# Kernel tuning notes

Hardware: AMD Instinct MI355X
Metric: run time of the kernel (lower is better)

The kernel has to match this reference:

```python
import jax, jax.numpy as jnp
import numpy as np
from jax import lax

L = 2048        # leaves per tree
VOCAB = 50000
IN_DIM = 300
MEM = 150
HID = 50
NCLS = 5


def _balanced_tree(n_leaf):
    # children-before-parent topological order; node ids: [0, n_leaf) leaves,
    # [n_leaf, 2*n_leaf-1) internal, last id is the root's single child (ROOT is passthrough).
    level = list(range(n_leaf)); nid = n_leaf; lefts = []; rights = []
    while len(level) > 1:
        nxt = []
        for j in range(0, len(level) - 1, 2):
            lefts.append(level[j]); rights.append(level[j + 1]); nxt.append(nid); nid += 1
        if len(level) % 2:
            nxt.append(level[-1])
        level = nxt
    return np.asarray(lefts, np.int32), np.asarray(rights, np.int32)


def setup_inputs() -> dict:
    key = jax.random.key(0)
    ks = jax.random.split(key, 12)
    left, right = _balanced_tree(L)
    s = 0.05
    return {
        "l_tokens": jax.random.randint(ks[0], (L,), 0, VOCAB, dtype=jnp.int32),
        "r_tokens": jax.random.randint(ks[1], (L,), 0, VOCAB, dtype=jnp.int32),
        "left_idx": jnp.asarray(left),
        "right_idx": jnp.asarray(right),
        "emb": jax.random.normal(ks[2], (VOCAB, IN_DIM), jnp.float32) * s,
        "W_ioux": jax.random.normal(ks[3], (IN_DIM, 3 * MEM), jnp.float32) * s,
        "b_ioux": jnp.zeros((3 * MEM,), jnp.float32),
        "W_iouh": jax.random.normal(ks[4], (MEM, 3 * MEM), jnp.float32) * s,
        "b_iouh": jnp.zeros((3 * MEM,), jnp.float32),
        "W_fx": jax.random.normal(ks[5], (IN_DIM, MEM), jnp.float32) * s,
        "b_fx": jnp.zeros((MEM,), jnp.float32),
        "W_fh": jax.random.normal(ks[6], (MEM, MEM), jnp.float32) * s,
        "b_fh": jnp.zeros((MEM,), jnp.float32),
        "W_attn": jax.random.normal(ks[7], (2 * MEM, MEM), jnp.float32) * s,
        "b_attn": jnp.zeros((MEM,), jnp.float32),
        "W_wh": jax.random.normal(ks[8], (2 * MEM, HID), jnp.float32) * s,
        "b_wh": jnp.zeros((HID,), jnp.float32),
        "W_wp": jax.random.normal(ks[9], (HID, NCLS), jnp.float32) * s,
        "b_wp": jnp.zeros((NCLS,), jnp.float32),
    }


def _gates(iou):
    i, o, u = jnp.split(iou, 3, axis=-1)
    return jax.nn.sigmoid(i), jax.nn.sigmoid(o), jnp.tanh(u)


def _tree_lstm(tokens, left, right, emb, W_ioux, b_ioux, W_iouh, b_iouh, W_fh, b_fh):
    # Leaves (child_c = child_h = 0): iou = ioux(x) + iouh(0); fc term vanishes.
    x = emb[tokens]                                   # [L, in_dim]
    i, o, u = _gates(x @ W_ioux + b_ioux + b_iouh)
    c_leaf = i * u
    h_leaf = o * jnp.tanh(c_leaf)
    n_leaf = tokens.shape[0]
    N = 2 * n_leaf - 1
    C = jnp.zeros((N, MEM), x.dtype).at[:n_leaf].set(c_leaf)
    H = jnp.zeros((N, MEM), x.dtype).at[:n_leaf].set(h_leaf)

    # Internal nodes (inputs=None branch): iou = iouh(sum h_child); f_k = sigmoid(fh(h_k)).
    def step(carry, inp):
        C, H = carry
        k, li, ri = inp
        hl, hr = H[li], H[ri]
        i, o, u = _gates((hl + hr) @ W_iouh + b_iouh)
        fl = jax.nn.sigmoid(hl @ W_fh + b_fh)
        fr = jax.nn.sigmoid(hr @ W_fh + b_fh)
        c = i * u + fl * C[li] + fr * C[ri]
        h = o * jnp.tanh(c)
        return (C.at[k].set(c), H.at[k].set(h)), None

    ids = jnp.arange(n_leaf, N, dtype=jnp.int32)
    (C, H), _ = lax.scan(step, (C, H), (ids, left, right))
    return H  # [N, MEM]; H[-1] is the root hidden state (ROOT is passthrough)


def reference(l_tokens, r_tokens, left_idx, right_idx, emb, W_ioux, b_ioux, W_iouh, b_iouh, W_fx, b_fx, W_fh, b_fh, W_attn, b_attn, W_wh, b_wh, W_wp, b_wp):
    Hl = _tree_lstm(l_tokens, left_idx, right_idx, emb, W_ioux, b_ioux, W_iouh, b_iouh, W_fh, b_fh)
    Hr = _tree_lstm(r_tokens, left_idx, right_idx, emb, W_ioux, b_ioux, W_iouh, b_iouh, W_fh, b_fh)
    # Soft cross-attention over all node hidden states (torch code builds [Nr,Nl,m] beta;
    # here expressed as matmuls -- identical math).
    scores = Hl @ Hr.T                               # [Nl, Nr]
    beta_sum = jax.nn.softmax(scores, axis=1) @ Hr    # [Nl, MEM]
    alpha_sum = jax.nn.softmax(scores.T, axis=1) @ Hl  # [Nr, MEM]
    v_l = jnp.concatenate([Hl, beta_sum], axis=1) @ W_attn + b_attn
    v_r = jnp.concatenate([Hr, alpha_sum], axis=1) @ W_attn + b_attn
    lh = v_l[-1:]  # root hidden (root_idx is the root's matched row)
    rh = v_r[-1:]
    feats = jnp.concatenate([lh * rh, jnp.abs(lh - rh)], axis=1)
    hid = jax.nn.sigmoid(feats @ W_wh + b_wh)
    return jax.nn.log_softmax(hid @ W_wp + b_wp, axis=-1)  # [1, NCLS]
```

## Files before the change

### kernel.cpp

```cpp
#include <hip/hip_runtime.h>
#include <math.h>

#define LEAVES 2048
#define NN     4095
#define MEMD   150
#define IOUD   450
#define IND    300
#define STR    152
#define CT     4096


__device__ __forceinline__ float sigf(float x) { return 1.f / (1.f + expf(-x)); }

__global__ __launch_bounds__(640) void k_leaf(
    const int* __restrict__ ltok, const int* __restrict__ rtok,
    const float* __restrict__ emb, const float* __restrict__ Wx,
    const float* __restrict__ bx, const float* __restrict__ bh,
    float* __restrict__ C, float* __restrict__ H)
{
    __shared__ float xs[IND][8];
    __shared__ int   tok[8];
    __shared__ float pb[300][13];
    const int tree = blockIdx.y, t = threadIdx.x;
    const int leaf0 = blockIdx.x << 3;
    const int* toks = tree ? rtok : ltok;

    if (t < 8) tok[t] = toks[leaf0 + t];
    __syncthreads();
    if (t < 600) {
        int q = t >> 3, m = t & 7;
        float4 v = *(const float4*)(emb + (size_t)tok[m] * IND + 4 * q);
        xs[4*q+0][m] = v.x; xs[4*q+1][m] = v.y;
        xs[4*q+2][m] = v.z; xs[4*q+3][m] = v.w;
    }
    __syncthreads();

    const int kh = (t >= 320) ? 1 : 0;
    const int tt = t - 320 * kh;
    const bool act = (tt < 300);
    const int hf = (tt >= 150) ? 1 : 0;
    const int d  = tt - 150 * hf;
    const int m0 = hf * 4;

    float ai[4], ao[4], au[4];
    if (act) {
        if (kh == 0) {
            const float bi = bx[d]       + bh[d];
            const float bo = bx[d + 150] + bh[d + 150];
            const float bu = bx[d + 300] + bh[d + 300];
            #pragma unroll
            for (int m = 0; m < 4; ++m) { ai[m] = bi; ao[m] = bo; au[m] = bu; }
        } else {
            #pragma unroll
            for (int m = 0; m < 4; ++m) { ai[m] = 0.f; ao[m] = 0.f; au[m] = 0.f; }
        }
        const float* wp = Wx + d;
        const int kb = kh * 150;
        #pragma unroll 5
        for (int kk = 0; kk < 150; ++kk) {
            const int k = kb + kk;
            float wi = wp[k * IOUD];
            float wo = wp[k * IOUD + 150];
            float wu = wp[k * IOUD + 300];
            float4 x4 = *(const float4*)(&xs[k][m0]);
            float xv[4] = {x4.x, x4.y, x4.z, x4.w};
            #pragma unroll
            for (int m = 0; m < 4; ++m) {
                ai[m] = fmaf(xv[m], wi, ai[m]);
                ao[m] = fmaf(xv[m], wo, ao[m]);
                au[m] = fmaf(xv[m], wu, au[m]);
            }
        }
    }
    if (kh == 1 && act) {
        #pragma unroll
        for (int m = 0; m < 4; ++m) {
            pb[tt][3*m + 0] = ai[m];
            pb[tt][3*m + 1] = ao[m];
            pb[tt][3*m + 2] = au[m];
        }
    }
    __syncthreads();
    if (kh == 0 && act) {
        float* Ct = C + ((size_t)tree * CT + leaf0 + m0) * STR;
        float* Ht = H + ((size_t)tree * CT + leaf0 + m0) * STR;
        #pragma unroll
        for (int m = 0; m < 4; ++m) {
            float aiv = ai[m] + pb[tt][3*m + 0];
            float aov = ao[m] + pb[tt][3*m + 1];
            float auv = au[m] + pb[tt][3*m + 2];
            float c = sigf(aiv) * tanhf(auv);
            float h = sigf(aov) * tanhf(c);
            Ct[(size_t)m * STR + d] = c;
            Ht[(size_t)m * STR + d] = h;
        }
    }
}

__global__ __launch_bounds__(640) void k_lvl(
    const float* __restrict__ Wh, const float* __restrict__ bh,
    const float* __restrict__ Wf, const float* __restrict__ bf,
    float* __restrict__ C, float* __restrict__ H, int PB, int CB)
{
    __shared__ float buf[MEMD][8];
    __shared__ float pb[300][11];
    const int tree = blockIdx.y, t = threadIdx.x;
    const int p0 = blockIdx.x * 4;
    float* Ct = C + (size_t)tree * CT * STR;
    float* Ht = H + (size_t)tree * CT * STR;

    if (t < 600) {
        int m = t / 150, d2 = t - m * 150;
        int cc = CB + 2 * (p0 + m);
        float a = Ht[(size_t)cc * STR + d2];
        float b = Ht[(size_t)(cc + 1) * STR + d2];
        buf[d2][2*m + 0] = a + b;
        buf[d2][2*m + 1] = a;
    }
    __syncthreads();

    const int kh = (t >= 320) ? 1 : 0;
    const int tt = t - 320 * kh;
    const bool act = (tt < 300);
    const int hf = (tt >= 150) ? 1 : 0;
    const int d  = tt - 150 * hf;
    const int m0 = hf * 2;

    float ai[2], ao[2], au[2], afs[2], afl[2], cl[2], cr[2];
    if (act) {
        if (kh == 0) {
            const float bi = bh[d], bo = bh[d + 150], bu = bh[d + 300], bfv = bf[d];
            #pragma unroll
            for (int m = 0; m < 2; ++m) {
                ai[m] = bi; ao[m] = bo; au[m] = bu;
                afs[m] = 2.f * bfv; afl[m] = bfv;
                int cc = CB + 2 * (p0 + m0 + m);
                cl[m] = Ct[(size_t)cc * STR + d];
                cr[m] = Ct[(size_t)(cc + 1) * STR + d];
            }
        } else {
            #pragma unroll
            for (int m = 0; m < 2; ++m) {
                ai[m] = 0.f; ao[m] = 0.f; au[m] = 0.f; afs[m] = 0.f; afl[m] = 0.f;
            }
        }
        const float* whp = Wh + d;
        const float* wfp = Wf + d;
        const int kb = kh * 75;
        #pragma unroll 5
        for (int kk = 0; kk < 75; ++kk) {
            const int k = kb + kk;
            float wi = whp[k * IOUD];
            float wo = whp[k * IOUD + 150];
            float wu = whp[k * IOUD + 300];
            float wf = wfp[k * MEMD];
            float4 p4 = *(const float4*)(&buf[k][2 * m0]);
            float hs0 = p4.x, hl0 = p4.y, hs1 = p4.z, hl1 = p4.w;
            ai[0]  = fmaf(hs0, wi, ai[0]);   ai[1]  = fmaf(hs1, wi, ai[1]);
            ao[0]  = fmaf(hs0, wo, ao[0]);   ao[1]  = fmaf(hs1, wo, ao[1]);
            au[0]  = fmaf(hs0, wu, au[0]);   au[1]  = fmaf(hs1, wu, au[1]);
            afs[0] = fmaf(hs0, wf, afs[0]);  afs[1] = fmaf(hs1, wf, afs[1]);
            afl[0] = fmaf(hl0, wf, afl[0]);  afl[1] = fmaf(hl1, wf, afl[1]);
        }
    }
    if (kh == 1 && act) {
        #pragma unroll
        for (int m = 0; m < 2; ++m) {
            pb[tt][5*m + 0] = ai[m];
            pb[tt][5*m + 1] = ao[m];
            pb[tt][5*m + 2] = au[m];
            pb[tt][5*m + 3] = afs[m];
            pb[tt][5*m + 4] = afl[m];
        }
    }
    __syncthreads();
    if (kh == 0 && act) {
        #pragma unroll
        for (int m = 0; m < 2; ++m) {
            float aiv  = ai[m]  + pb[tt][5*m + 0];
            float aov  = ao[m]  + pb[tt][5*m + 1];
            float auv  = au[m]  + pb[tt][5*m + 2];
            float afsv = afs[m] + pb[tt][5*m + 3];
            float aflv = afl[m] + pb[tt][5*m + 4];
            float frv = afsv - aflv;
            float c = sigf(aiv) * tanhf(auv) + sigf(aflv) * cl[m] + sigf(frv) * cr[m];
            float h = sigf(aov) * tanhf(c);
            size_t rw = (size_t)(PB + p0 + m0 + m) * STR + d;
            Ct[rw] = c;
            Ht[rw] = h;
        }
    }
}

__global__ __launch_bounds__(640) void k_node(
    const float* __restrict__ Wh, const float* __restrict__ bh,
    const float* __restrict__ Wf, const float* __restrict__ bf,
    float* __restrict__ C, float* __restrict__ H, int PB, int CB)
{
    __shared__ float hsv[MEMD], hlv[MEMD];
    __shared__ float part[4][5][152];
    const int tree = blockIdx.y, node = blockIdx.x, t = threadIdx.x;
    float* Ct = C + (size_t)tree * CT * STR;
    float* Ht = H + (size_t)tree * CT * STR;
    const int c0 = CB + 2 * node;

    if (t < MEMD) {
        float a = Ht[(size_t)c0 * STR + t];
        float b = Ht[(size_t)(c0 + 1) * STR + t];
        hsv[t] = a + b;
        hlv[t] = a;
    }
    __syncthreads();

    const int grp = t / 160, d = t - grp * 160;
    if (d < MEMD) {
        const int k0 = (grp * MEMD) >> 2;
        const int k1 = ((grp + 1) * MEMD) >> 2;
        float ai = 0.f, ao = 0.f, au = 0.f, afs = 0.f, afl = 0.f;
        const float* whp = Wh + d;
        const float* wfp = Wf + d;
        #pragma unroll 4
        for (int k = k0; k < k1; ++k) {
            float wi = whp[k * IOUD];
            float wo = whp[k * IOUD + 150];
            float wu = whp[k * IOUD + 300];
            float wf = wfp[k * MEMD];
            float hs = hsv[k], hl = hlv[k];
            ai  = fmaf(hs, wi, ai);
            ao  = fmaf(hs, wo, ao);
            au  = fmaf(hs, wu, au);
            afs = fmaf(hs, wf, afs);
            afl = fmaf(hl, wf, afl);
        }
        part[grp][0][d] = ai;  part[grp][1][d] = ao;  part[grp][2][d] = au;
        part[grp][3][d] = afs; part[grp][4][d] = afl;
    }
    __syncthreads();

    if (t < MEMD) {
        const int d2 = t;
        float ai = bh[d2], ao = bh[d2 + 150], au = bh[d2 + 300];
        float bfv = bf[d2];
        float afs = 2.f * bfv, afl = bfv;
        #pragma unroll
        for (int g = 0; g < 4; ++g) {
            ai  += part[g][0][d2]; ao  += part[g][1][d2]; au += part[g][2][d2];
            afs += part[g][3][d2]; afl += part[g][4][d2];
        }
        float cl = Ct[(size_t)c0 * STR + d2];
        float cr = Ct[(size_t)(c0 + 1) * STR + d2];
        float frv = afs - afl;
        float c = sigf(ai) * tanhf(au) + sigf(afl) * cl + sigf(frv) * cr;
        float h = sigf(ao) * tanhf(c);
        size_t rw = (size_t)(PB + node) * STR + d2;
        Ct[rw] = c;
        Ht[rw] = h;
    }
}

__global__ __launch_bounds__(256) void k_attn(
    const float* __restrict__ H, float* __restrict__ cstat, float* __restrict__ part)
{
    __shared__ float lv[MEMD];
    __shared__ float sc[64];
    __shared__ float pv[64];
    const int bid = blockIdx.x, t = threadIdx.x;
    const int side = bid >> 6, chunk = bid & 63;
    const int j0 = chunk << 6;
    const int jn = min(64, NN - j0);
    const float* lastrow = H + ((size_t)side * CT + (NN - 1)) * STR;
    if (t < MEMD) lv[t] = lastrow[t];
    __syncthreads();

    const float* src = H + (size_t)(side ^ 1) * CT * STR + (size_t)j0 * STR;
    const int wave = t >> 6, lane = t & 63;
    for (int r = wave; r < jn; r += 4) {
        const float* row = src + (size_t)r * STR;
        float a = lv[lane] * row[lane] + lv[lane + 64] * row[lane + 64];
        if (lane < 22) a += lv[lane + 128] * row[lane + 128];
        #pragma unroll
        for (int off = 32; off; off >>= 1) a += __shfl_xor(a, off);
        if (lane == 0) sc[r] = a;
    }
    __syncthreads();
    if (wave == 0) {
        float v = (lane < jn) ? sc[lane] : -3.4e38f;
        float m = v;
        #pragma unroll
        for (int off = 32; off; off >>= 1) m = fmaxf(m, __shfl_xor(m, off));
        float e = (lane < jn) ? expf(v - m) : 0.f;
        pv[lane] = e;
        float s = e;
        #pragma unroll
        for (int off = 32; off; off >>= 1) s += __shfl_xor(s, off);
        if (lane == 0) {
            cstat[(side * 64 + chunk) * 2 + 0] = m;
            cstat[(side * 64 + chunk) * 2 + 1] = s;
        }
    }
    __syncthreads();
    if (t < MEMD) {
        float a = 0.f;
        for (int j = 0; j < jn; ++j) a += pv[j] * src[(size_t)j * STR + t];
        part[(size_t)(side * 64 + chunk) * STR + t] = a;
    }
}

__global__ __launch_bounds__(512) void k_final(
    const float* __restrict__ H, const float* __restrict__ cstat,
    const float* __restrict__ part,
    const float* __restrict__ Wattn, const float* __restrict__ battn,
    const float* __restrict__ Wwh, const float* __restrict__ bwh,
    const float* __restrict__ Wwp, const float* __restrict__ bwp,
    float* __restrict__ outp)
{
    __shared__ float scl[2][64];
    __shared__ float gseS[2];
    __shared__ float ba[300], catl[300], catr[300], vl[150], vr[150];
    __shared__ float feats[300], hid[50], logits[5];
    const int t = threadIdx.x, wave = t >> 6, lane = t & 63;

    if (wave < 2) {
        float lm = cstat[(wave * 64 + lane) * 2 + 0];
        float ls = cstat[(wave * 64 + lane) * 2 + 1];
        float m = lm;
        #pragma unroll
        for (int off = 32; off; off >>= 1) m = fmaxf(m, __shfl_xor(m, off));
        float s = expf(lm - m);
        scl[wave][lane] = s;
        float se = ls * s;
        #pragma unroll
        for (int off = 32; off; off >>= 1) se += __shfl_xor(se, off);
        if (lane == 0) gseS[wave] = se;
    }
    __syncthreads();
    if (t < 300) {
        int side = t / MEMD, d = t - side * MEMD;
        float a = 0.f;
        for (int c = 0; c < 64; ++c)
            a += part[(size_t)(side * 64 + c) * STR + d] * scl[side][c];
        ba[t] = a / gseS[side];
    }
    __syncthreads();
    const float* Hl_last = H + (size_t)(0 * CT + NN - 1) * STR;
    const float* Hr_last = H + (size_t)(1 * CT + NN - 1) * STR;
    if (t < MEMD) {
        catl[t] = Hl_last[t]; catl[150 + t] = ba[t];
        catr[t] = Hr_last[t]; catr[150 + t] = ba[150 + t];
    }
    __syncthreads();
    if (t < 300) {
        int d = (t < 150) ? t : t - 150;
        const float* cat = (t < 150) ? catl : catr;
        float a = battn[d];
        for (int k = 0; k < 300; ++k) a = fmaf(cat[k], Wattn[k * 150 + d], a);
        if (t < 150) vl[d] = a; else vr[d] = a;
    }
    __syncthreads();
    if (t < MEMD) {
        feats[t] = vl[t] * vr[t];
        feats[150 + t] = fabsf(vl[t] - vr[t]);
    }
    __syncthreads();
    if (t < 50) {
        float a = bwh[t];
        for (int k = 0; k < 300; ++k) a = fmaf(feats[k], Wwh[k * 50 + t], a);
        hid[t] = sigf(a);
    }
    __syncthreads();
    if (t < 5) {
        float a = bwp[t];
        for (int g = 0; g < 50; ++g) a = fmaf(hid[g], Wwp[g * 5 + t], a);
        logits[t] = a;
    }
    __syncthreads();
    if (t == 0) {
        float m = logits[0];
        for (int c = 1; c < 5; ++c) m = fmaxf(m, logits[c]);
        float s = 0.f;
        for (int c = 0; c < 5; ++c) s += expf(logits[c] - m);
        float lse = m + logf(s);
        for (int c = 0; c < 5; ++c) outp[c] = logits[c] - lse;
    }
}

extern "C" void kernel_launch(void* const* d_in, const int* in_sizes, int n_in,
                              void* d_out, int out_size, void* d_ws, size_t ws_size,
                              hipStream_t stream)
{
    const int*   ltok  = (const int*)d_in[0];
    const int*   rtok  = (const int*)d_in[1];
    const float* emb   = (const float*)d_in[4];
    const float* Wx    = (const float*)d_in[5];
    const float* bx    = (const float*)d_in[6];
    const float* Wh    = (const float*)d_in[7];
    const float* bh    = (const float*)d_in[8];
    const float* Wf    = (const float*)d_in[11];
    const float* bf    = (const float*)d_in[12];
    const float* Wattn = (const float*)d_in[13];
    const float* battn = (const float*)d_in[14];
    const float* Wwh   = (const float*)d_in[15];
    const float* bwh   = (const float*)d_in[16];
    const float* Wwp   = (const float*)d_in[17];
    const float* bwp   = (const float*)d_in[18];
    float* out = (float*)d_out;

    float* ws   = (float*)d_ws;
    float* C    = ws;
    float* H    = C + (size_t)2 * CT * STR;
    float* cs   = H + (size_t)2 * CT * STR;
    float* part = cs + 256;

    k_leaf<<<dim3(256, 2), dim3(640), 0, stream>>>(ltok, rtok, emb, Wx, bx, bh, C, H);

    k_lvl<<<dim3(256, 2), dim3(640), 0, stream>>>(Wh, bh, Wf, bf, C, H, 2048, 0);
    k_lvl<<<dim3(128, 2), dim3(640), 0, stream>>>(Wh, bh, Wf, bf, C, H, 3072, 2048);
    k_lvl<<<dim3(64,  2), dim3(640), 0, stream>>>(Wh, bh, Wf, bf, C, H, 3584, 3072);

    k_node<<<dim3(128, 2), dim3(640), 0, stream>>>(Wh, bh, Wf, bf, C, H, 3840, 3584);
    k_node<<<dim3(64,  2), dim3(640), 0, stream>>>(Wh, bh, Wf, bf, C, H, 3968, 3840);
    k_node<<<dim3(32,  2), dim3(640), 0, stream>>>(Wh, bh, Wf, bf, C, H, 4032, 3968);
    k_node<<<dim3(16,  2), dim3(640), 0, stream>>>(Wh, bh, Wf, bf, C, H, 4064, 4032);
    k_node<<<dim3(8,   2), dim3(640), 0, stream>>>(Wh, bh, Wf, bf, C, H, 4080, 4064);
    k_node<<<dim3(4,   2), dim3(640), 0, stream>>>(Wh, bh, Wf, bf, C, H, 4088, 4080);
    k_node<<<dim3(2,   2), dim3(640), 0, stream>>>(Wh, bh, Wf, bf, C, H, 4092, 4088);
    k_node<<<dim3(1,   2), dim3(640), 0, stream>>>(Wh, bh, Wf, bf, C, H, 4094, 4092);

    k_attn<<<dim3(128), dim3(256), 0, stream>>>(H, cs, part);
    k_final<<<dim3(1), dim3(512), 0, stream>>>(H, cs, part, Wattn, battn,
                                               Wwh, bwh, Wwp, bwp, out);
}
```

Measured before the change: 150.9 us.

## Split leaf/level reductions four ways with float2 columns and templated parents-per-block

The leaf and level kernels now split the K reduction across four thread groups instead of two. Each thread handles two adjacent output columns through float2 weight loads and stores, and partial sums are combined through a larger shared buffer. k_lvl is templated on parents per block so the second level runs with one parent per block across more blocks, and the third level moves to k_node with one block per node, raising block count at the shallow levels. This costs more shared-memory traffic in the combine step, and each block reuses its weights over fewer nodes.

New measurement: 182.7 us. +21.1%, slower.

```diff
diff --git a/kernel.cpp b/kernel.cpp
--- a/kernel.cpp
+++ b/kernel.cpp
@@ -18,9 +18,9 @@
     const float* __restrict__ bx, const float* __restrict__ bh,
     float* __restrict__ C, float* __restrict__ H)
 {
-    __shared__ float xs[IND][8];
-    __shared__ int   tok[8];
-    __shared__ float pb[300][13];
+    __shared__ float  xs[IND][8];
+    __shared__ int    tok[8];
+    __shared__ float2 pb[3][150][13];
     const int tree = blockIdx.y, t = threadIdx.x;
     const int leaf0 = blockIdx.x << 3;
     const int* toks = tree ? rtok : ltok;
@@ -35,82 +35,103 @@
     }
     __syncthreads();
 
-    const int kh = (t >= 320) ? 1 : 0;
-    const int tt = t - 320 * kh;
-    const bool act = (tt < 300);
-    const int hf = (tt >= 150) ? 1 : 0;
-    const int d  = tt - 150 * hf;
+    const bool act = (t < 600);
+    const int kh = t / 150;
+    const int tt = t - kh * 150;
+    const int hf = tt / 75;
+    const int dq = tt - hf * 75;
+    const int d0 = 2 * dq;
     const int m0 = hf * 4;
 
-    float ai[4], ao[4], au[4];
+    float2 Ai[4], Ao[4], Au[4];
     if (act) {
         if (kh == 0) {
-            const float bi = bx[d]       + bh[d];
-            const float bo = bx[d + 150] + bh[d + 150];
-            const float bu = bx[d + 300] + bh[d + 300];
-            #pragma unroll
-            for (int m = 0; m < 4; ++m) { ai[m] = bi; ao[m] = bo; au[m] = bu; }
+            float2 bi, bo, bu;
+            bi.x = bx[d0]       + bh[d0];       bi.y = bx[d0+1]     + bh[d0+1];
+            bo.x = bx[d0 + 150] + bh[d0 + 150]; bo.y = bx[d0+151]   + bh[d0+151];
+            bu.x = bx[d0 + 300] + bh[d0 + 300]; bu.y = bx[d0+301]   + bh[d0+301];
+            #pragma unroll
+            for (int m = 0; m < 4; ++m) { Ai[m] = bi; Ao[m] = bo; Au[m] = bu; }
         } else {
             #pragma unroll
-            for (int m = 0; m < 4; ++m) { ai[m] = 0.f; ao[m] = 0.f; au[m] = 0.f; }
-        }
-        const float* wp = Wx + d;
-        const int kb = kh * 150;
+            for (int m = 0; m < 4; ++m) {
+                Ai[m].x = 0.f; Ai[m].y = 0.f;
+                Ao[m].x = 0.f; Ao[m].y = 0.f;
+                Au[m].x = 0.f; Au[m].y = 0.f;
+            }
+        }
+        const int kb = kh * 75;
         #pragma unroll 5
-        for (int kk = 0; kk < 150; ++kk) {
+        for (int kk = 0; kk < 75; ++kk) {
             const int k = kb + kk;
-            float wi = wp[k * IOUD];
-            float wo = wp[k * IOUD + 150];
-            float wu = wp[k * IOUD + 300];
+            const float* wr = Wx + k * IOUD + d0;
+            float2 wi = *(const float2*)(wr);
+            float2 wo = *(const float2*)(wr + 150);
+            float2 wu = *(const float2*)(wr + 300);
             float4 x4 = *(const float4*)(&xs[k][m0]);
             float xv[4] = {x4.x, x4.y, x4.z, x4.w};
             #pragma unroll
             for (int m = 0; m < 4; ++m) {
-                ai[m] = fmaf(xv[m], wi, ai[m]);
-                ao[m] = fmaf(xv[m], wo, ao[m]);
-                au[m] = fmaf(xv[m], wu, au[m]);
-            }
-        }
-    }
-    if (kh == 1 && act) {
+                Ai[m].x = fmaf(xv[m], wi.x, Ai[m].x);
+                Ai[m].y = fmaf(xv[m], wi.y, Ai[m].y);
+                Ao[m].x = fmaf(xv[m], wo.x, Ao[m].x);
+                Ao[m].y = fmaf(xv[m], wo.y, Ao[m].y);
+                Au[m].x = fmaf(xv[m], wu.x, Au[m].x);
+                Au[m].y = fmaf(xv[m], wu.y, Au[m].y);
+            }
+        }
+    }
+    if (act && kh > 0) {
         #pragma unroll
         for (int m = 0; m < 4; ++m) {
-            pb[tt][3*m + 0] = ai[m];
-            pb[tt][3*m + 1] = ao[m];
-            pb[tt][3*m + 2] = au[m];
-        }
-    }
-    __syncthreads();
-    if (kh == 0 && act) {
+            pb[kh-1][tt][3*m + 0] = Ai[m];
+            pb[kh-1][tt][3*m + 1] = Ao[m];
+            pb[kh-1][tt][3*m + 2] = Au[m];
+        }
+    }
+    __syncthreads();
+    if (act && kh == 0) {
         float* Ct = C + ((size_t)tree * CT + leaf0 + m0) * STR;
         float* Ht = H + ((size_t)tree * CT + leaf0 + m0) * STR;
         #pragma unroll
         for (int m = 0; m < 4; ++m) {
-            float aiv = ai[m] + pb[tt][3*m + 0];
-            float aov = ao[m] + pb[tt][3*m + 1];
-            float auv = au[m] + pb[tt][3*m + 2];
-            float c = sigf(aiv) * tanhf(auv);
-            float h = sigf(aov) * tanhf(c);
-            Ct[(size_t)m * STR + d] = c;
-            Ht[(size_t)m * STR + d] = h;
-        }
-    }
-}
-
+            float2 ai = Ai[m], ao = Ao[m], au = Au[m];
+            #pragma unroll
+            for (int g = 0; g < 3; ++g) {
+                float2 p0v = pb[g][tt][3*m + 0];
+                float2 p1v = pb[g][tt][3*m + 1];
+                float2 p2v = pb[g][tt][3*m + 2];
+                ai.x += p0v.x; ai.y += p0v.y;
+                ao.x += p1v.x; ao.y += p1v.y;
+                au.x += p2v.x; au.y += p2v.y;
+            }
+            float c0 = sigf(ai.x) * tanhf(au.x);
+            float h0 = sigf(ao.x) * tanhf(c0);
+            float c1 = sigf(ai.y) * tanhf(au.y);
+            float h1 = sigf(ao.y) * tanhf(c1);
+            float2 cc; cc.x = c0; cc.y = c1;
+            float2 hh; hh.x = h0; hh.y = h1;
+            *(float2*)(Ct + (size_t)m * STR + d0) = cc;
+            *(float2*)(Ht + (size_t)m * STR + d0) = hh;
+        }
+    }
+}
+
+template<int P>
 __global__ __launch_bounds__(640) void k_lvl(
     const float* __restrict__ Wh, const float* __restrict__ bh,
     const float* __restrict__ Wf, const float* __restrict__ bf,
     float* __restrict__ C, float* __restrict__ H, int PB, int CB)
 {
-    __shared__ float buf[MEMD][8];
-    __shared__ float pb[300][11];
+    __shared__ float  buf[MEMD][4 * P];
+    __shared__ float2 pb[3][150][5 * P + 1];
     const int tree = blockIdx.y, t = threadIdx.x;
-    const int p0 = blockIdx.x * 4;
+    const int p0 = blockIdx.x * 2 * P;
     float* Ct = C + (size_t)tree * CT * STR;
     float* Ht = H + (size_t)tree * CT * STR;
 
-    if (t < 600) {
-        int m = t / 150, d2 = t - m * 150;
+    if (t < 2 * P * MEMD) {
+        int m = t / MEMD, d2 = t - m * MEMD;
         int cc = CB + 2 * (p0 + m);
         float a = Ht[(size_t)cc * STR + d2];
         float b = Ht[(size_t)(cc + 1) * STR + d2];
@@ -119,75 +140,98 @@
     }
     __syncthreads();
 
-    const int kh = (t >= 320) ? 1 : 0;
-    const int tt = t - 320 * kh;
-    const bool act = (tt < 300);
-    const int hf = (tt >= 150) ? 1 : 0;
-    const int d  = tt - 150 * hf;
-    const int m0 = hf * 2;
-
-    float ai[2], ao[2], au[2], afs[2], afl[2], cl[2], cr[2];
+    const bool act = (t < 600);
+    const int kh = t / 150;
+    const int tt = t - kh * 150;
+    const int hf = tt / 75;
+    const int dq = tt - hf * 75;
+    const int d0 = 2 * dq;
+    const int m0 = hf * P;
+
+    float2 Ai[P], Ao[P], Au[P], Afs[P], Afl[P];
     if (act) {
         if (kh == 0) {
-            const float bi = bh[d], bo = bh[d + 150], bu = bh[d + 300], bfv = bf[d];
-            #pragma unroll
-            for (int m = 0; m < 2; ++m) {
-                ai[m] = bi; ao[m] = bo; au[m] = bu;
-                afs[m] = 2.f * bfv; afl[m] = bfv;
-                int cc = CB + 2 * (p0 + m0 + m);
-                cl[m] = Ct[(size_t)cc * STR + d];
-                cr[m] = Ct[(size_t)(cc + 1) * STR + d];
+            float2 bi, bo, bu, bfv;
+            bi.x = bh[d0];        bi.y = bh[d0 + 1];
+            bo.x = bh[d0 + 150];  bo.y = bh[d0 + 151];
+            bu.x = bh[d0 + 300];  bu.y = bh[d0 + 301];
+            bfv.x = bf[d0];       bfv.y = bf[d0 + 1];
+            #pragma unroll
+            for (int m = 0; m < P; ++m) {
+                Ai[m] = bi; Ao[m] = bo; Au[m] = bu;
+                Afs[m].x = 2.f * bfv.x; Afs[m].y = 2.f * bfv.y;
+                Afl[m] = bfv;
             }
         } else {
             #pragma unroll
-            for (int m = 0; m < 2; ++m) {
-                ai[m] = 0.f; ao[m] = 0.f; au[m] = 0.f; afs[m] = 0.f; afl[m] = 0.f;
-            }
-        }
-        const float* whp = Wh + d;
-        const float* wfp = Wf + d;
-        const int kb = kh * 75;
-        #pragma unroll 5
-        for (int kk = 0; kk < 75; ++kk) {
-            const int k = kb + kk;
-            float wi = whp[k * IOUD];
-            float wo = whp[k * IOUD + 150];
-            float wu = whp[k * IOUD + 300];
-            float wf = wfp[k * MEMD];
-            float4 p4 = *(const float4*)(&buf[k][2 * m0]);
-            float hs0 = p4.x, hl0 = p4.y, hs1 = p4.z, hl1 = p4.w;
-            ai[0]  = fmaf(hs0, wi, ai[0]);   ai[1]  = fmaf(hs1, wi, ai[1]);
-            ao[0]  = fmaf(hs0, wo, ao[0]);   ao[1]  = fmaf(hs1, wo, ao[1]);
-            au[0]  = fmaf(hs0, wu, au[0]);   au[1]  = fmaf(hs1, wu, au[1]);
-            afs[0] = fmaf(hs0, wf, afs[0]);  afs[1] = fmaf(hs1, wf, afs[1]);
-            afl[0] = fmaf(hl0, wf, afl[0]);  afl[1] = fmaf(hl1, wf, afl[1]);
-        }
-    }
-    if (kh == 1 && act) {
-        #pragma unroll
-        for (int m = 0; m < 2; ++m) {
-            pb[tt][5*m + 0] = ai[m];
-            pb[tt][5*m + 1] = ao[m];
-            pb[tt][5*m + 2] = au[m];
-            pb[tt][5*m + 3] = afs[m];
-            pb[tt][5*m + 4] = afl[m];
-        }
-    }
-    __syncthreads();
-    if (kh == 0 && act) {
-        #pragma unroll
-        for (int m = 0; m < 2; ++m) {
-            float aiv  = ai[m]  + pb[tt][5*m + 0];
-            float aov  = ao[m]  + pb[tt][5*m + 1];
-            float auv  = au[m]  + pb[tt][5*m + 2];
-            float afsv = afs[m] + pb[tt][5*m + 3];
-            float aflv = afl[m] + pb[tt][5*m + 4];
-            float frv = afsv - aflv;
-            float c = sigf(aiv) * tanhf(auv) + sigf(aflv) * cl[m] + sigf(frv) * cr[m];
-            float h = sigf(aov) * tanhf(c);
-            size_t rw = (size_t)(PB + p0 + m0 + m) * STR + d;
-            Ct[rw] = c;
-            Ht[rw] = h;
+            for (int m = 0; m < P; ++m) {
+                Ai[m].x = Ai[m].y = 0.f; Ao[m].x = Ao[m].y = 0.f;
+                Au[m].x = Au[m].y = 0.f; Afs[m].x = Afs[m].y = 0.f;
+                Afl[m].x = Afl[m].y = 0.f;
+            }
+        }
+        const int k0 = (kh * MEMD) >> 2;
+        const int k1 = ((kh + 1) * MEMD) >> 2;
+        #pragma unroll 4
+        for (int k = k0; k < k1; ++k) {
+            const float* wr = Wh + k * IOUD + d0;
+            float2 wi = *(const float2*)(wr);
+            float2 wo = *(const float2*)(wr + 150);
+            float2 wu = *(const float2*)(wr + 300);
+            float2 wf = *(const float2*)(Wf + k * MEMD + d0);
+            #pragma unroll
+            for (int m = 0; m < P; ++m) {
+                float2 pr = *(const float2*)(&buf[k][2 * (m0 + m)]);
+                float hs = pr.x, hl = pr.y;
+                Ai[m].x  = fmaf(hs, wi.x, Ai[m].x);   Ai[m].y  = fmaf(hs, wi.y, Ai[m].y);
+                Ao[m].x  = fmaf(hs, wo.x, Ao[m].x);   Ao[m].y  = fmaf(hs, wo.y, Ao[m].y);
+                Au[m].x  = fmaf(hs, wu.x, Au[m].x);   Au[m].y  = fmaf(hs, wu.y, Au[m].y);
+                Afs[m].x = fmaf(hs, wf.x, Afs[m].x);  Afs[m].y = fmaf(hs, wf.y, Afs[m].y);
+                Afl[m].x = fmaf(hl, wf.x, Afl[m].x);  Afl[m].y = fmaf(hl, wf.y, Afl[m].y);
+            }
+        }
+    }
+    if (act && kh > 0) {
+        #pragma unroll
+        for (int m = 0; m < P; ++m) {
+            pb[kh-1][tt][5*m + 0] = Ai[m];
+            pb[kh-1][tt][5*m + 1] = Ao[m];
+            pb[kh-1][tt][5*m + 2] = Au[m];
+            pb[kh-1][tt][5*m + 3] = Afs[m];
+            pb[kh-1][tt][5*m + 4] = Afl[m];
+        }
+    }
+    __syncthreads();
+    if (act && kh == 0) {
+        #pragma unroll
+        for (int m = 0; m < P; ++m) {
+            float2 ai = Ai[m], ao = Ao[m], au = Au[m], afs = Afs[m], afl = Afl[m];
+            #pragma unroll
+            for (int g = 0; g < 3; ++g) {
+                float2 q0 = pb[g][tt][5*m + 0];
+                float2 q1 = pb[g][tt][5*m + 1];
+                float2 q2 = pb[g][tt][5*m + 2];
+                float2 q3 = pb[g][tt][5*m + 3];
+                float2 q4 = pb[g][tt][5*m + 4];
+                ai.x += q0.x; ai.y += q0.y;
+                ao.x += q1.x; ao.y += q1.y;
+                au.x += q2.x; au.y += q2.y;
+                afs.x += q3.x; afs.y += q3.y;
+                afl.x += q4.x; afl.y += q4.y;
+            }
+            int p = p0 + m0 + m;
+            int cc = CB + 2 * p;
+            float2 cl = *(const float2*)(Ct + (size_t)cc * STR + d0);
+            float2 cr = *(const float2*)(Ct + (size_t)(cc + 1) * STR + d0);
+            float fr0 = afs.x - afl.x, fr1 = afs.y - afl.y;
+            float c0 = sigf(ai.x) * tanhf(au.x) + sigf(afl.x) * cl.x + sigf(fr0) * cr.x;
+            float h0 = sigf(ao.x) * tanhf(c0);
+            float c1 = sigf(ai.y) * tanhf(au.y) + sigf(afl.y) * cl.y + sigf(fr1) * cr.y;
+            float h1 = sigf(ao.y) * tanhf(c1);
+            float2 cc2; cc2.x = c0; cc2.y = c1;
+            float2 hh2; hh2.x = h0; hh2.y = h1;
+            *(float2*)(Ct + (size_t)(PB + p) * STR + d0) = cc2;
+            *(float2*)(Ht + (size_t)(PB + p) * STR + d0) = hh2;
         }
     }
 }
@@ -413,10 +457,10 @@
 
     k_leaf<<<dim3(256, 2), dim3(640), 0, stream>>>(ltok, rtok, emb, Wx, bx, bh, C, H);
 
-    k_lvl<<<dim3(256, 2), dim3(640), 0, stream>>>(Wh, bh, Wf, bf, C, H, 2048, 0);
-    k_lvl<<<dim3(128, 2), dim3(640), 0, stream>>>(Wh, bh, Wf, bf, C, H, 3072, 2048);
-    k_lvl<<<dim3(64,  2), dim3(640), 0, stream>>>(Wh, bh, Wf, bf, C, H, 3584, 3072);
-
+    k_lvl<2><<<dim3(256, 2), dim3(640), 0, stream>>>(Wh, bh, Wf, bf, C, H, 2048, 0);
+    k_lvl<1><<<dim3(256, 2), dim3(640), 0, stream>>>(Wh, bh, Wf, bf, C, H, 3072, 2048);
+
+    k_node<<<dim3(256, 2), dim3(640), 0, stream>>>(Wh, bh, Wf, bf, C, H, 3584, 3072);
     k_node<<<dim3(128, 2), dim3(640), 0, stream>>>(Wh, bh, Wf, bf, C, H, 3840, 3584);
     k_node<<<dim3(64,  2), dim3(640), 0, stream>>>(Wh, bh, Wf, bf, C, H, 3968, 3840);
     k_node<<<dim3(32,  2), dim3(640), 0, stream>>>(Wh, bh, Wf, bf, C, H, 4032, 3968);
```

## Fuse top tree levels into one persistent kernel with global barriers

Applied to the files above, without the earlier changes.

Replaces the seven small per-level node launches for the top of the tree with a single persistent kernel of 128 blocks. The blocks synchronise between levels through atomic counters in workspace, which a new zero kernel resets at the start of each call. The leaf and level kernels are also reworked to 320 threads, each covering all 8 or NP parents instead of splitting them across half-blocks. The third level now uses k_node instead of k_lvl. The changes aim to cut launch overhead and raise reuse of each weight load, at the cost of spin-wait barriers that rely on all 128 blocks being resident at once, and lower occupancy.

New measurement: 234.5 us. 55.4% more time.

```diff
diff --git a/kernel.cpp b/kernel.cpp
--- a/kernel.cpp
+++ b/kernel.cpp
@@ -12,7 +12,12 @@
 
 __device__ __forceinline__ float sigf(float x) { return 1.f / (1.f + expf(-x)); }
 
-__global__ __launch_bounds__(640) void k_leaf(
+__global__ void k_zero(int* __restrict__ flags)
+{
+    if (threadIdx.x < 8) flags[threadIdx.x] = 0;
+}
+
+__global__ __launch_bounds__(320) void k_leaf(
     const int* __restrict__ ltok, const int* __restrict__ rtok,
     const float* __restrict__ emb, const float* __restrict__ Wx,
     const float* __restrict__ bx, const float* __restrict__ bh,
@@ -20,39 +25,36 @@
 {
     __shared__ float xs[IND][8];
     __shared__ int   tok[8];
-    __shared__ float pb[300][13];
+    __shared__ float pb[MEMD][25];
     const int tree = blockIdx.y, t = threadIdx.x;
     const int leaf0 = blockIdx.x << 3;
     const int* toks = tree ? rtok : ltok;
 
     if (t < 8) tok[t] = toks[leaf0 + t];
     __syncthreads();
-    if (t < 600) {
-        int q = t >> 3, m = t & 7;
+    for (int idx = t; idx < 600; idx += 320) {
+        int q = idx >> 3, m = idx & 7;
         float4 v = *(const float4*)(emb + (size_t)tok[m] * IND + 4 * q);
         xs[4*q+0][m] = v.x; xs[4*q+1][m] = v.y;
         xs[4*q+2][m] = v.z; xs[4*q+3][m] = v.w;
     }
     __syncthreads();
 
-    const int kh = (t >= 320) ? 1 : 0;
-    const int tt = t - 320 * kh;
-    const bool act = (tt < 300);
-    const int hf = (tt >= 150) ? 1 : 0;
-    const int d  = tt - 150 * hf;
-    const int m0 = hf * 4;
-
-    float ai[4], ao[4], au[4];
+    const bool act = (t < 300);
+    const int kh = t / 150;
+    const int d  = t - kh * 150;
+
+    float ai[8], ao[8], au[8];
     if (act) {
         if (kh == 0) {
             const float bi = bx[d]       + bh[d];
             const float bo = bx[d + 150] + bh[d + 150];
             const float bu = bx[d + 300] + bh[d + 300];
             #pragma unroll
-            for (int m = 0; m < 4; ++m) { ai[m] = bi; ao[m] = bo; au[m] = bu; }
+            for (int m = 0; m < 8; ++m) { ai[m] = bi; ao[m] = bo; au[m] = bu; }
         } else {
             #pragma unroll
-            for (int m = 0; m < 4; ++m) { ai[m] = 0.f; ao[m] = 0.f; au[m] = 0.f; }
+            for (int m = 0; m < 8; ++m) { ai[m] = 0.f; ao[m] = 0.f; au[m] = 0.f; }
         }
         const float* wp = Wx + d;
         const int kb = kh * 150;
@@ -62,33 +64,34 @@
             float wi = wp[k * IOUD];
             float wo = wp[k * IOUD + 150];
             float wu = wp[k * IOUD + 300];
-            float4 x4 = *(const float4*)(&xs[k][m0]);
-            float xv[4] = {x4.x, x4.y, x4.z, x4.w};
-            #pragma unroll
-            for (int m = 0; m < 4; ++m) {
+            float4 x0 = *(const float4*)(&xs[k][0]);
+            float4 x1 = *(const float4*)(&xs[k][4]);
+            float xv[8] = {x0.x, x0.y, x0.z, x0.w, x1.x, x1.y, x1.z, x1.w};
+            #pragma unroll
+            for (int m = 0; m < 8; ++m) {
                 ai[m] = fmaf(xv[m], wi, ai[m]);
                 ao[m] = fmaf(xv[m], wo, ao[m]);
                 au[m] = fmaf(xv[m], wu, au[m]);
             }
         }
     }
-    if (kh == 1 && act) {
-        #pragma unroll
-        for (int m = 0; m < 4; ++m) {
-            pb[tt][3*m + 0] = ai[m];
-            pb[tt][3*m + 1] = ao[m];
-            pb[tt][3*m + 2] = au[m];
-        }
-    }
-    __syncthreads();
-    if (kh == 0 && act) {
-        float* Ct = C + ((size_t)tree * CT + leaf0 + m0) * STR;
-        float* Ht = H + ((size_t)tree * CT + leaf0 + m0) * STR;
-        #pragma unroll
-        for (int m = 0; m < 4; ++m) {
-            float aiv = ai[m] + pb[tt][3*m + 0];
-            float aov = ao[m] + pb[tt][3*m + 1];
-            float auv = au[m] + pb[tt][3*m + 2];
+    if (act && kh == 1) {
+        #pragma unroll
+        for (int m = 0; m < 8; ++m) {
+            pb[d][3*m + 0] = ai[m];
+            pb[d][3*m + 1] = ao[m];
+            pb[d][3*m + 2] = au[m];
+        }
+    }
+    __syncthreads();
+    if (act && kh == 0) {
+        float* Ct = C + ((size_t)tree * CT + leaf0) * STR;
+        float* Ht = H + ((size_t)tree * CT + leaf0) * STR;
+        #pragma unroll
+        for (int m = 0; m < 8; ++m) {
+            float aiv = ai[m] + pb[d][3*m + 0];
+            float aov = ao[m] + pb[d][3*m + 1];
+            float auv = au[m] + pb[d][3*m + 2];
             float c = sigf(aiv) * tanhf(auv);
             float h = sigf(aov) * tanhf(c);
             Ct[(size_t)m * STR + d] = c;
@@ -97,20 +100,21 @@
     }
 }
 
-__global__ __launch_bounds__(640) void k_lvl(
+template<int NP>
+__global__ __launch_bounds__(320) void k_lvl(
     const float* __restrict__ Wh, const float* __restrict__ bh,
     const float* __restrict__ Wf, const float* __restrict__ bf,
     float* __restrict__ C, float* __restrict__ H, int PB, int CB)
 {
-    __shared__ float buf[MEMD][8];
-    __shared__ float pb[300][11];
+    __shared__ float buf[MEMD][2 * NP];
+    __shared__ float pb[MEMD][5 * NP + 1];
     const int tree = blockIdx.y, t = threadIdx.x;
-    const int p0 = blockIdx.x * 4;
+    const int p0 = blockIdx.x * NP;
     float* Ct = C + (size_t)tree * CT * STR;
     float* Ht = H + (size_t)tree * CT * STR;
 
-    if (t < 600) {
-        int m = t / 150, d2 = t - m * 150;
+    for (int idx = t; idx < NP * MEMD; idx += 320) {
+        int m = idx / MEMD, d2 = idx - m * MEMD;
         int cc = CB + 2 * (p0 + m);
         float a = Ht[(size_t)cc * STR + d2];
         float b = Ht[(size_t)(cc + 1) * STR + d2];
@@ -119,28 +123,25 @@
     }
     __syncthreads();
 
-    const int kh = (t >= 320) ? 1 : 0;
-    const int tt = t - 320 * kh;
-    const bool act = (tt < 300);
-    const int hf = (tt >= 150) ? 1 : 0;
-    const int d  = tt - 150 * hf;
-    const int m0 = hf * 2;
-
-    float ai[2], ao[2], au[2], afs[2], afl[2], cl[2], cr[2];
+    const bool act = (t < 300);
+    const int kh = t / 150;
+    const int d  = t - kh * 150;
+
+    float ai[NP], ao[NP], au[NP], afs[NP], afl[NP], cl[NP], cr[NP];
     if (act) {
         if (kh == 0) {
             const float bi = bh[d], bo = bh[d + 150], bu = bh[d + 300], bfv = bf[d];
             #pragma unroll
-            for (int m = 0; m < 2; ++m) {
+            for (int m = 0; m < NP; ++m) {
                 ai[m] = bi; ao[m] = bo; au[m] = bu;
                 afs[m] = 2.f * bfv; afl[m] = bfv;
-                int cc = CB + 2 * (p0 + m0 + m);
+                int cc = CB + 2 * (p0 + m);
                 cl[m] = Ct[(size_t)cc * STR + d];
                 cr[m] = Ct[(size_t)(cc + 1) * STR + d];
             }
         } else {
             #pragma unroll
-            for (int m = 0; m < 2; ++m) {
+            for (int m = 0; m < NP; ++m) {
                 ai[m] = 0.f; ao[m] = 0.f; au[m] = 0.f; afs[m] = 0.f; afl[m] = 0.f;
             }
         }
@@ -154,56 +155,60 @@
             float wo = whp[k * IOUD + 150];
             float wu = whp[k * IOUD + 300];
             float wf = wfp[k * MEMD];
-            float4 p4 = *(const float4*)(&buf[k][2 * m0]);
-            float hs0 = p4.x, hl0 = p4.y, hs1 = p4.z, hl1 = p4.w;
-            ai[0]  = fmaf(hs0, wi, ai[0]);   ai[1]  = fmaf(hs1, wi, ai[1]);
-            ao[0]  = fmaf(hs0, wo, ao[0]);   ao[1]  = fmaf(hs1, wo, ao[1]);
-            au[0]  = fmaf(hs0, wu, au[0]);   au[1]  = fmaf(hs1, wu, au[1]);
-            afs[0] = fmaf(hs0, wf, afs[0]);  afs[1] = fmaf(hs1, wf, afs[1]);
-            afl[0] = fmaf(hl0, wf, afl[0]);  afl[1] = fmaf(hl1, wf, afl[1]);
-        }
-    }
-    if (kh == 1 && act) {
-        #pragma unroll
-        for (int m = 0; m < 2; ++m) {
-            pb[tt][5*m + 0] = ai[m];
-            pb[tt][5*m + 1] = ao[m];
-            pb[tt][5*m + 2] = au[m];
-            pb[tt][5*m + 3] = afs[m];
-            pb[tt][5*m + 4] = afl[m];
-        }
-    }
-    __syncthreads();
-    if (kh == 0 && act) {
-        #pragma unroll
-        for (int m = 0; m < 2; ++m) {
-            float aiv  = ai[m]  + pb[tt][5*m + 0];
-            float aov  = ao[m]  + pb[tt][5*m + 1];
-            float auv  = au[m]  + pb[tt][5*m + 2];
-            float afsv = afs[m] + pb[tt][5*m + 3];
-            float aflv = afl[m] + pb[tt][5*m + 4];
+            #pragma unroll
+            for (int m2 = 0; m2 < NP; m2 += 2) {
+                float4 p4 = *(const float4*)(&buf[k][2 * m2]);
+                float hs0 = p4.x, hl0 = p4.y, hs1 = p4.z, hl1 = p4.w;
+                ai[m2]    = fmaf(hs0, wi, ai[m2]);
+                ai[m2+1]  = fmaf(hs1, wi, ai[m2+1]);
+                ao[m2]    = fmaf(hs0, wo, ao[m2]);
+                ao[m2+1]  = fmaf(hs1, wo, ao[m2+1]);
+                au[m2]    = fmaf(hs0, wu, au[m2]);
+                au[m2+1]  = fmaf(hs1, wu, au[m2+1]);
+                afs[m2]   = fmaf(hs0, wf, afs[m2]);
+                afs[m2+1] = fmaf(hs1, wf, afs[m2+1]);
+                afl[m2]   = fmaf(hl0, wf, afl[m2]);
+                afl[m2+1] = fmaf(hl1, wf, afl[m2+1]);
+            }
+        }
+    }
+    if (act && kh == 1) {
+        #pragma unroll
+        for (int m = 0; m < NP; ++m) {
+            pb[d][5*m + 0] = ai[m];
+            pb[d][5*m + 1] = ao[m];
+            pb[d][5*m + 2] = au[m];
+            pb[d][5*m + 3] = afs[m];
+            pb[d][5*m + 4] = afl[m];
+        }
+    }
+    __syncthreads();
+    if (act && kh == 0) {
+        #pragma unroll
+        for (int m = 0; m < NP; ++m) {
+            float aiv  = ai[m]  + pb[d][5*m + 0];
+            float aov  = ao[m]  + pb[d][5*m + 1];
+            float auv  = au[m]  + pb[d][5*m + 2];
+            float afsv = afs[m] + pb[d][5*m + 3];
+            float aflv = afl[m] + pb[d][5*m + 4];
             float frv = afsv - aflv;
             float c = sigf(aiv) * tanhf(auv) + sigf(aflv) * cl[m] + sigf(frv) * cr[m];
             float h = sigf(aov) * tanhf(c);
-            size_t rw = (size_t)(PB + p0 + m0 + m) * STR + d;
+            size_t rw = (size_t)(PB + p0 + m) * STR + d;
             Ct[rw] = c;
             Ht[rw] = h;
         }
     }
 }
 
-__global__ __launch_bounds__(640) void k_node(
+__device__ __forceinline__ void node_body(
     const float* __restrict__ Wh, const float* __restrict__ bh,
     const float* __restrict__ Wf, const float* __restrict__ bf,
-    float* __restrict__ C, float* __restrict__ H, int PB, int CB)
-{
-    __shared__ float hsv[MEMD], hlv[MEMD];
-    __shared__ float part[4][5][152];
-    const int tree = blockIdx.y, node = blockIdx.x, t = threadIdx.x;
-    float* Ct = C + (size_t)tree * CT * STR;
-    float* Ht = H + (size_t)tree * CT * STR;
+    float* __restrict__ Ct, float* __restrict__ Ht,
+    float (*hsv), float (*hlv), float (*part)[5][152],
+    int node, int PB, int CB, int t)
+{
     const int c0 = CB + 2 * node;
-
     if (t < MEMD) {
         float a = Ht[(size_t)c0 * STR + t];
         float b = Ht[(size_t)(c0 + 1) * STR + t];
@@ -211,7 +216,6 @@
         hlv[t] = a;
     }
     __syncthreads();
-
     const int grp = t / 160, d = t - grp * 160;
     if (d < MEMD) {
         const int k0 = (grp * MEMD) >> 2;
@@ -236,7 +240,6 @@
         part[grp][3][d] = afs; part[grp][4][d] = afl;
     }
     __syncthreads();
-
     if (t < MEMD) {
         const int d2 = t;
         float ai = bh[d2], ao = bh[d2 + 150], au = bh[d2 + 300];
@@ -255,6 +258,53 @@
         size_t rw = (size_t)(PB + node) * STR + d2;
         Ct[rw] = c;
         Ht[rw] = h;
+    }
+}
+
+__global__ __launch_bounds__(640) void k_node(
+    const float* __restrict__ Wh, const float* __restrict__ bh,
+    const float* __restrict__ Wf, const float* __restrict__ bf,
+    float* __restrict__ C, float* __restrict__ H, int PB, int CB)
+{
+    __shared__ float hsv[MEMD], hlv[MEMD];
+    __shared__ float part[4][5][152];
+    const int tree = blockIdx.y;
+    float* Ct = C + (size_t)tree * CT * STR;
+    float* Ht = H + (size_t)tree * CT * STR;
+    node_body(Wh, bh, Wf, bf, Ct, Ht, hsv, hlv, part,
+              blockIdx.x, PB, CB, threadIdx.x);
+}
+
+__global__ __launch_bounds__(640) void k_tail(
+    const float* __restrict__ Wh, const float* __restrict__ bh,
+    const float* __restrict__ Wf, const float* __restrict__ bf,
+    float* __restrict__ C, float* __restrict__ H, int* __restrict__ flags)
+{
+    __shared__ float hsv[MEMD], hlv[MEMD];
+    __shared__ float part[4][5][152];
+    const int tree = blockIdx.y, b = blockIdx.x, t = threadIdx.x;
+    float* Ct = C + (size_t)tree * CT * STR;
+    float* Ht = H + (size_t)tree * CT * STR;
+
+    const int ns[7] = {64, 32, 16, 8, 4, 2, 1};
+    const int pbs[7] = {3968, 4032, 4064, 4080, 4088, 4092, 4094};
+    const int cbs[7] = {3840, 3968, 4032, 4064, 4080, 4088, 4092};
+
+    #pragma unroll 1
+    for (int l = 0; l < 7; ++l) {
+        if (b < ns[l]) {
+            node_body(Wh, bh, Wf, bf, Ct, Ht, hsv, hlv, part, b, pbs[l], cbs[l], t);
+        }
+        if (l < 6) {
+            __syncthreads();
+            if (t == 0) {
+                __threadfence();
+                atomicAdd(&flags[l], 1);
+                while (__hip_atomic_load(&flags[l], __ATOMIC_ACQUIRE,
+                                         __HIP_MEMORY_SCOPE_AGENT) < 128) {}
+            }
+            __syncthreads();
+        }
     }
 }
 
@@ -410,21 +460,19 @@
     float* H    = C + (size_t)2 * CT * STR;
     float* cs   = H + (size_t)2 * CT * STR;
     float* part = cs + 256;
-
-    k_leaf<<<dim3(256, 2), dim3(640), 0, stream>>>(ltok, rtok, emb, Wx, bx, bh, C, H);
-
-    k_lvl<<<dim3(256, 2), dim3(640), 0, stream>>>(Wh, bh, Wf, bf, C, H, 2048, 0);
-    k_lvl<<<dim3(128, 2), dim3(640), 0, stream>>>(Wh, bh, Wf, bf, C, H, 3072, 2048);
-    k_lvl<<<dim3(64,  2), dim3(640), 0, stream>>>(Wh, bh, Wf, bf, C, H, 3584, 3072);
-
+    int*   flags = (int*)(part + (size_t)128 * STR);
+
+    k_zero<<<dim3(1), dim3(64), 0, stream>>>(flags);
+
+    k_leaf<<<dim3(256, 2), dim3(320), 0, stream>>>(ltok, rtok, emb, Wx, bx, bh, C, H);
+
+    k_lvl<4><<<dim3(256, 2), dim3(320), 0, stream>>>(Wh, bh, Wf, bf, C, H, 2048, 0);
+    k_lvl<2><<<dim3(256, 2), dim3(320), 0, stream>>>(Wh, bh, Wf, bf, C, H, 3072, 2048);
+
+    k_node<<<dim3(256, 2), dim3(640), 0, stream>>>(Wh, bh, Wf, bf, C, H, 3584, 3072);
     k_node<<<dim3(128, 2), dim3(640), 0, stream>>>(Wh, bh, Wf, bf, C, H, 3840, 3584);
-    k_node<<<dim3(64,  2), dim3(640), 0, stream>>>(Wh, bh, Wf, bf, C, H, 3968, 3840);
-    k_node<<<dim3(32,  2), dim3(640), 0, stream>>>(Wh, bh, Wf, bf, C, H, 4032, 3968);
-    k_node<<<dim3(16,  2), dim3(640), 0, stream>>>(Wh, bh, Wf, bf, C, H, 4064, 4032);
-    k_node<<<dim3(8,   2), dim3(640), 0, stream>>>(Wh, bh, Wf, bf, C, H, 4080, 4064);
-    k_node<<<dim3(4,   2), dim3(640), 0, stream>>>(Wh, bh, Wf, bf, C, H, 4088, 4080);
-    k_node<<<dim3(2,   2), dim3(640), 0, stream>>>(Wh, bh, Wf, bf, C, H, 4092, 4088);
-    k_node<<<dim3(1,   2), dim3(640), 0, stream>>>(Wh, bh, Wf, bf, C, H, 4094, 4092);
+
+    k_tail<<<dim3(64, 2), dim3(640), 0, stream>>>(Wh, bh, Wf, bf, C, H, flags);
 
     k_attn<<<dim3(128), dim3(256), 0, stream>>>(H, cs, part);
     k_final<<<dim3(1), dim3(512), 0, stream>>>(H, cs, part, Wattn, battn,
```
